# Optimization experiments

Hardware: AMD Instinct MI355X
Metric: run time of the kernel (lower is better)

Reference implementation:

```python
import jax, jax.numpy as jnp
import numpy as np

B, T, F = 32, 64, 128          # batch, time_steps, input_dim
H = 8                           # feat_dim (GRU hidden, MHA embed)
NH, HD = 4, 2                   # num_heads, head_dim
HID = 32                        # hidden_dim (out_proj out-features)


def setup_inputs() -> dict:
    key = jax.random.key(0)
    ks = jax.random.split(key, 16)
    s = 0.1
    inp = {
        'x': jax.random.normal(ks[0], (B, T, F), jnp.float32),
        # input_proj: Linear(F, F)
        'Wp': jax.random.normal(ks[1], (F, F), jnp.float32) * s,
        'bp': jax.random.normal(ks[2], (F,), jnp.float32) * s,
        # per-feature GRU weights stacked over F (input size 1 -> squeeze)
        'W_ih': jax.random.normal(ks[3], (F, 3 * H), jnp.float32) * s,
        'b_ih': jax.random.normal(ks[4], (F, 3 * H), jnp.float32) * s,
        'W_hh': jax.random.normal(ks[5], (F, 3 * H, H), jnp.float32) * s,
        'b_hh': jax.random.normal(ks[6], (F, 3 * H), jnp.float32) * s,
        # shared MultiheadAttention (embed=H, heads=NH)
        'in_w': jax.random.normal(ks[7], (3 * H, H), jnp.float32) * s,
        'in_b': jax.random.normal(ks[8], (3 * H,), jnp.float32) * s,
        'ow': jax.random.normal(ks[9], (H, H), jnp.float32) * s,
        'ob': jax.random.normal(ks[10], (H,), jnp.float32) * s,
        # out_proj: Linear(F*H, HID)
        'Wout': jax.random.normal(ks[11], (HID, F * H), jnp.float32) * s,
        'bout': jax.random.normal(ks[12], (HID,), jnp.float32) * s,
    }
    return inp


def _forward(x, Wp, bp, W_ih, b_ih, W_hh, b_hh, in_w, in_b, ow, ob, Wout, bout):
    xp = x @ Wp.T + bp                               # [B,T,F] input_proj

    # ---- batched per-feature GRU (vectorized over B and F, scan over T) ----
    def step(h, x_t):                                # h [B,F,H], x_t [B,F]
        gx = x_t[..., None] * W_ih + b_ih            # [B,F,3H]
        gh = jnp.einsum('bfh,fgh->bfg', h, W_hh) + b_hh
        r = jax.nn.sigmoid(gx[..., :H] + gh[..., :H])
        z = jax.nn.sigmoid(gx[..., H:2 * H] + gh[..., H:2 * H])
        n = jnp.tanh(gx[..., 2 * H:] + r * gh[..., 2 * H:])
        h_new = (1.0 - z) * n + z * h
        return h_new, h_new

    h0 = jnp.zeros((x.shape[0], F, H), x.dtype)
    _, hs = jax.lax.scan(step, h0, jnp.moveaxis(xp, 1, 0))   # [T,B,F,H]
    out = jnp.moveaxis(hs, 0, 1)                              # [B,T,F,H]

    # ---- shared MHA over time, batched across (B, F) ----
    seq = out.transpose(0, 2, 1, 3)                           # [B,F,T,H]
    qkv = seq @ in_w.T + in_b                                 # [B,F,T,3H]
    q, k, v = jnp.split(qkv, 3, axis=-1)
    def heads(t):  # [B,F,T,H] -> [B,F,T,NH,HD]
        return t.reshape(t.shape[:-1] + (NH, HD))
    q, k, v = heads(q), heads(k), heads(v)
    scale = 1.0 / np.sqrt(HD)
    scores = jnp.einsum('bfqnd,bfknd->bfnqk', q, k) * scale   # [B,F,NH,T,T]
    w = jax.nn.softmax(scores, axis=-1)
    ctx = jnp.einsum('bfnqk,bfknd->bfqnd', w, v)
    ctx = ctx.reshape(ctx.shape[:2] + (ctx.shape[2], H))      # [B,F,T,H]
    attn_out = ctx @ ow.T + ob                                # [B,F,T,H]
    attention = attn_out.transpose(0, 2, 1, 3)                # [B,T,F,H]

    # ---- flatten GRU outputs and project ----
    y = out.reshape(out.shape[0], out.shape[1], F * H) @ Wout.T + bout  # [B,T,HID]
    return y, attention


def reference(x, Wp, bp, W_ih, b_ih, W_hh, b_hh, in_w, in_b, ow, ob, Wout, bout):
    return _forward(x, Wp, bp, W_ih, b_ih, W_hh, b_hh, in_w, in_b, ow, ob, Wout, bout)
```

## Files before the change

### kernel.cpp

```cpp
#include <hip/hip_runtime.h>


namespace {
constexpr int Bb = 32, Tt = 64, Ff = 128, Hh = 8, HIDh = 32;
constexpr int G3H = 24;
constexpr float L2E = 1.44269504088896340736f;
constexpr int XPS  = 0;
constexpr int HOUT = 260;
constexpr int OCT  = 2340;
constexpr int KV   = 4900;
constexpr int SM_SIZE = KV + 4 * 1088;
}

__device__ __forceinline__ float rcp_(float x) {
#if __has_builtin(__builtin_amdgcn_rcpf)
  return __builtin_amdgcn_rcpf(x);
#else
  return 1.0f / x;
#endif
}
__device__ __forceinline__ float exp2_(float x) {
#if __has_builtin(__builtin_amdgcn_exp2f)
  return __builtin_amdgcn_exp2f(x);
#else
  return exp2f(x);
#endif
}

#define MHA_STEP(K0C, K1C, V0C, V1C)                         \
  {                                                          \
    _Pragma("unroll") for (int i = 0; i < 4; ++i) {          \
      float s = fmaf(q0[i], K0C, q1[i] * K1C);               \
      float p = exp2_(s);                                    \
      ps[i] += p;                                            \
      c0[i] = fmaf(p, V0C, c0[i]);                           \
      c1[i] = fmaf(p, V1C, c1[i]);                           \
    }                                                        \
  }

__global__ __launch_bounds__(256, 4) void k_fused(
    const float* __restrict__ x, const float* __restrict__ Wp, const float* __restrict__ bp,
    const float* __restrict__ W_ih, const float* __restrict__ b_ih,
    const float* __restrict__ W_hh, const float* __restrict__ b_hh,
    const float* __restrict__ in_w, const float* __restrict__ in_b,
    const float* __restrict__ ow, const float* __restrict__ ob,
    float* __restrict__ outp, float* __restrict__ attn) {
  __shared__ float smem[SM_SIZE];
  const int tid = threadIdx.x;
  const int t = tid & 63;
  const int w = tid >> 6;
  const int blk = blockIdx.x;
  const int b = blk >> 5;
  const int f0 = (blk & 31) * 4;

  {
    const int f = f0 + w;
    const float4* xr = (const float4*)(x + (b * Tt + t) * Ff);
    const float4* wr = (const float4*)(Wp + f * Ff);
    float acc = bp[f];
#pragma unroll 8
    for (int k = 0; k < Ff / 4; ++k) {
      float4 xv = xr[k], wv = wr[k];
      acc = fmaf(xv.x, wv.x, acc); acc = fmaf(xv.y, wv.y, acc);
      acc = fmaf(xv.z, wv.z, acc); acc = fmaf(xv.w, wv.w, acc);
    }
    smem[XPS + w * 65 + t] = acc;
  }
  __syncthreads();

  if (tid < 32) {
    __builtin_amdgcn_s_setprio(1);
    const int g = t >> 3, j = t & 7;
    const int f = f0 + g;
    const float* wb = W_hh + (f * G3H + j) * Hh;
    const float nL = -L2E, S2 = 2.0f * L2E;
    float w0s[8], w1s[8], w2s[8];
#pragma unroll
    for (int h = 0; h < 8; ++h) {
      w0s[h] = wb[h] * nL;
      w1s[h] = wb[64 + h] * nL;
      w2s[h] = wb[128 + h] * S2;
    }
    const float wi0s = W_ih[f * G3H + j] * nL;
    const float wi1s = W_ih[f * G3H + 8 + j] * nL;
    const float wi2s = W_ih[f * G3H + 16 + j] * S2;
    const float bias_r = (b_ih[f * G3H + j] + b_hh[f * G3H + j]) * nL;
    const float bias_z = (b_ih[f * G3H + 8 + j] + b_hh[f * G3H + 8 + j]) * nL;
    const float bi2s = b_ih[f * G3H + 16 + j] * S2;
    const float bh2s = b_hh[f * G3H + 16 + j] * S2;
    float hall[8];
#pragma unroll
    for (int h = 0; h < 8; ++h) hall[h] = 0.f;
    float h_own = 0.f;
    const int base = t & 56;
    float* hdst = &smem[HOUT + g * 520 + j * 65];
    const float* xps = &smem[XPS + g * 65];
    for (int tt = 0; tt < Tt; ++tt) {
      float xt = xps[tt];
      float a0 = bias_r, a1 = bias_z, a2 = bh2s;
#pragma unroll
      for (int h = 0; h < 8; ++h) {
        a0 = fmaf(hall[h], w0s[h], a0);
        a1 = fmaf(hall[h], w1s[h], a1);
        a2 = fmaf(hall[h], w2s[h], a2);
      }
      float r = rcp_(1.0f + exp2_(fmaf(xt, wi0s, a0)));
      float z = rcp_(1.0f + exp2_(fmaf(xt, wi1s, a1)));
      float narg = fmaf(r, a2, fmaf(xt, wi2s, bi2s));
      float n = fmaf(-2.0f, rcp_(exp2_(narg) + 1.0f), 1.0f);
      float hn = fmaf(z, h_own - n, n);
      hdst[tt] = hn;
      h_own = hn;
#pragma unroll
      for (int h = 0; h < 8; ++h) hall[h] = __shfl(hn, base + h, 64);
    }
    __builtin_amdgcn_s_setprio(0);
  }
  __syncthreads();

  {
    float4* og = (float4*)(outp + (size_t)(b * Ff + f0) * Tt * Hh);
#pragma unroll
    for (int i = 0; i < 2; ++i) {
      int v = i * 256 + tid;
      int fl = v >> 7, rem = v & 127;
      int tt = rem >> 1, j0 = (rem & 1) * 4;
      const float* hp = &smem[HOUT + fl * 520 + j0 * 65 + tt];
      og[v] = make_float4(hp[0], hp[65], hp[130], hp[195]);
    }
  }

  {
    constexpr float SCL = 0.70710678118654752f * L2E;
    const float* hsrc = &smem[HOUT + w * 520];
    float* oc = &smem[OCT + w * 640];
    float* kk0 = &smem[KV + w * 1088];
    float* kk1 = kk0 + 272;
    float* vv0 = kk0 + 544;
    float* vv1 = kk0 + 816;

    float sq[8];
#pragma unroll
    for (int h = 0; h < 8; ++h) sq[h] = hsrc[h * 65 + t];
    float qv[8], ka[8], va[8];
#pragma unroll
    for (int jj = 0; jj < 8; ++jj) {
      float aq = in_b[jj], ak = in_b[8 + jj], av = in_b[16 + jj];
#pragma unroll
      for (int h = 0; h < 8; ++h) {
        aq = fmaf(sq[h], in_w[jj * 8 + h], aq);
        ak = fmaf(sq[h], in_w[(8 + jj) * 8 + h], ak);
        av = fmaf(sq[h], in_w[(16 + jj) * 8 + h], av);
      }
      qv[jj] = aq * SCL; ka[jj] = ak; va[jj] = av;
    }
#pragma unroll
    for (int n = 0; n < 4; ++n) {
      *(float2*)&oc[t * 10 + 2 * n] = make_float2(qv[2 * n], qv[2 * n + 1]);
      kk0[n * 68 + t] = ka[2 * n];
      kk1[n * 68 + t] = ka[2 * n + 1];
      vv0[n * 68 + t] = va[2 * n];
      vv1[n * 68 + t] = va[2 * n + 1];
    }
    asm volatile("s_waitcnt lgkmcnt(0)" ::: "memory");

    const int n = t >> 4, qq = t & 15;
    float q0[4], q1[4];
#pragma unroll
    for (int i = 0; i < 4; ++i) {
      float2 qp = *(const float2*)&oc[(qq + 16 * i) * 10 + 2 * n];
      q0[i] = qp.x; q1[i] = qp.y;
    }
    float ps[4], c0[4], c1[4];
#pragma unroll
    for (int i = 0; i < 4; ++i) { ps[i] = 0.f; c0[i] = 0.f; c1[i] = 0.f; }
#pragma unroll 2
    for (int kt4 = 0; kt4 < Tt; kt4 += 4) {
      float4 k0 = *(const float4*)&kk0[n * 68 + kt4];
      float4 k1 = *(const float4*)&kk1[n * 68 + kt4];
      float4 v0 = *(const float4*)&vv0[n * 68 + kt4];
      float4 v1 = *(const float4*)&vv1[n * 68 + kt4];
      MHA_STEP(k0.x, k1.x, v0.x, v1.x)
      MHA_STEP(k0.y, k1.y, v0.y, v1.y)
      MHA_STEP(k0.z, k1.z, v0.z, v1.z)
      MHA_STEP(k0.w, k1.w, v0.w, v1.w)
    }
#pragma unroll
    for (int i = 0; i < 4; ++i) {
      float inv = rcp_(ps[i]);
      *(float2*)&oc[(qq + 16 * i) * 10 + 2 * n] =
          make_float2(c0[i] * inv, c1[i] * inv);
    }
    asm volatile("s_waitcnt lgkmcnt(0)" ::: "memory");

    {
      float2 cp0 = *(const float2*)&oc[t * 10 + 0];
      float2 cp1 = *(const float2*)&oc[t * 10 + 2];
      float2 cp2 = *(const float2*)&oc[t * 10 + 4];
      float2 cp3 = *(const float2*)&oc[t * 10 + 6];
      float cx[8] = {cp0.x, cp0.y, cp1.x, cp1.y, cp2.x, cp2.y, cp3.x, cp3.y};
      float o8[8];
#pragma unroll
      for (int jj = 0; jj < 8; ++jj) {
        float a = ob[jj];
#pragma unroll
        for (int h = 0; h < 8; ++h) a = fmaf(cx[h], ow[jj * 8 + h], a);
        o8[jj] = a;
      }
      *(float2*)&oc[t * 10 + 0] = make_float2(o8[0], o8[1]);
      *(float2*)&oc[t * 10 + 2] = make_float2(o8[2], o8[3]);
      *(float2*)&oc[t * 10 + 4] = make_float2(o8[4], o8[5]);
      *(float2*)&oc[t * 10 + 6] = make_float2(o8[6], o8[7]);
    }
  }
  __syncthreads();

  {
#pragma unroll
    for (int i = 0; i < 2; ++i) {
      int v = i * 256 + tid;
      int tt = v >> 3, c = v & 7;
      int fl = c >> 1, h0 = (c & 1) * 4;
      const float* sp = &smem[OCT + fl * 640 + tt * 10 + h0];
      float4 val = make_float4(sp[0], sp[1], sp[2], sp[3]);
      *(float4*)(attn + (((size_t)b * Tt + tt) * Ff + f0 + fl) * Hh + h0) = val;
    }
  }
}

__global__ __launch_bounds__(128) void k_outproj(
    const float* __restrict__ outp, const float* __restrict__ Wout,
    const float* __restrict__ bout, float* __restrict__ y) {
  constexpr int TT = 8;
  int blk = blockIdx.x;
  int b = blk >> 3;
  int t0 = (blk & 7) * TT;
  int tid = threadIdx.x;
  int oq = tid >> 4;
  int fc = tid & 15;
  float acc[TT][4];
#pragma unroll
  for (int tt = 0; tt < TT; ++tt)
#pragma unroll
    for (int od = 0; od < 4; ++od) acc[tt][od] = 0.f;
#pragma unroll
  for (int ff = 0; ff < 8; ++ff) {
    int f = fc * 8 + ff;
    const float4* rb = (const float4*)(outp + ((b * Ff + f) * Tt + t0) * Hh);
    float4 rv[16];
#pragma unroll
    for (int i = 0; i < 16; ++i) rv[i] = rb[i];
#pragma unroll
    for (int od = 0; od < 4; ++od) {
      int o = oq * 4 + od;
      const float4* wbp = (const float4*)(Wout + o * (Ff * Hh) + f * Hh);
      float4 wa = wbp[0], wc = wbp[1];
#pragma unroll
      for (int tt = 0; tt < TT; ++tt) {
        float4 ra = rv[tt * 2], rc = rv[tt * 2 + 1];
        float s = acc[tt][od];
        s = fmaf(ra.x, wa.x, s); s = fmaf(ra.y, wa.y, s);
        s = fmaf(ra.z, wa.z, s); s = fmaf(ra.w, wa.w, s);
        s = fmaf(rc.x, wc.x, s); s = fmaf(rc.y, wc.y, s);
        s = fmaf(rc.z, wc.z, s); s = fmaf(rc.w, wc.w, s);
        acc[tt][od] = s;
      }
    }
  }
#pragma unroll
  for (int tt = 0; tt < TT; ++tt)
#pragma unroll
    for (int od = 0; od < 4; ++od) {
      float v = acc[tt][od];
      v += __shfl_xor(v, 1, 16);
      v += __shfl_xor(v, 2, 16);
      v += __shfl_xor(v, 4, 16);
      v += __shfl_xor(v, 8, 16);
      acc[tt][od] = v;
    }
#pragma unroll
  for (int tt = 0; tt < TT; ++tt) {
    if (fc == tt) {
#pragma unroll
      for (int od = 0; od < 4; ++od) {
        int o = oq * 4 + od;
        y[(b * Tt + t0 + tt) * HIDh + o] = acc[tt][od] + bout[o];
      }
    }
  }
}

extern "C" void kernel_launch(void* const* d_in, const int* in_sizes, int n_in,
                              void* d_out, int out_size, void* d_ws, size_t ws_size,
                              hipStream_t stream) {
  (void)in_sizes; (void)n_in; (void)out_size; (void)ws_size;
  const float* x    = (const float*)d_in[0];
  const float* Wp   = (const float*)d_in[1];
  const float* bp   = (const float*)d_in[2];
  const float* W_ih = (const float*)d_in[3];
  const float* b_ih = (const float*)d_in[4];
  const float* W_hh = (const float*)d_in[5];
  const float* b_hh = (const float*)d_in[6];
  const float* in_w = (const float*)d_in[7];
  const float* in_b = (const float*)d_in[8];
  const float* ow   = (const float*)d_in[9];
  const float* ob   = (const float*)d_in[10];
  const float* Wout = (const float*)d_in[11];
  const float* bout = (const float*)d_in[12];

  float* y    = (float*)d_out;
  float* attn = (float*)d_out + Bb * Tt * HIDh;
  float* outp = (float*)d_ws;

  hipLaunchKernelGGL(k_fused, dim3(Bb * (Ff / 4)), dim3(256), 0, stream,
                     x, Wp, bp, W_ih, b_ih, W_hh, b_hh, in_w, in_b, ow, ob, outp, attn);
  hipLaunchKernelGGL(k_outproj, dim3(Bb * (Tt / 8)), dim3(128), 0, stream,
                     outp, Wout, bout, y);
}
```

Before: 61.93 us.

## Fuse output projection into main kernel via atomic accumulation

```diff
diff --git a/kernel.cpp b/kernel.cpp
--- a/kernel.cpp
+++ b/kernel.cpp
@@ -44,7 +44,8 @@
     const float* __restrict__ W_hh, const float* __restrict__ b_hh,
     const float* __restrict__ in_w, const float* __restrict__ in_b,
     const float* __restrict__ ow, const float* __restrict__ ob,
-    float* __restrict__ outp, float* __restrict__ attn) {
+    const float* __restrict__ Wout, const float* __restrict__ bout,
+    float* __restrict__ y, float* __restrict__ attn) {
   __shared__ float smem[SM_SIZE];
   const int tid = threadIdx.x;
   const int t = tid & 63;
@@ -119,15 +120,34 @@
   __syncthreads();
 
   {
-    float4* og = (float4*)(outp + (size_t)(b * Ff + f0) * Tt * Hh);
-#pragma unroll
-    for (int i = 0; i < 2; ++i) {
-      int v = i * 256 + tid;
-      int fl = v >> 7, rem = v & 127;
-      int tt = rem >> 1, j0 = (rem & 1) * 4;
-      const float* hp = &smem[HOUT + fl * 520 + j0 * 65 + tt];
-      og[v] = make_float4(hp[0], hp[65], hp[130], hp[195]);
-    }
+    const int od0 = w * 8;
+    float part[8];
+#pragma unroll
+    for (int od = 0; od < 8; ++od) part[od] = 0.f;
+#pragma unroll
+    for (int fl = 0; fl < 4; ++fl) {
+      float hv[8];
+#pragma unroll
+      for (int h = 0; h < 8; ++h) hv[h] = smem[HOUT + fl * 520 + h * 65 + t];
+#pragma unroll
+      for (int od = 0; od < 8; ++od) {
+        const float4* wq = (const float4*)(Wout + (od0 + od) * (Ff * Hh) + (f0 + fl) * Hh);
+        float4 wa = wq[0], wb4 = wq[1];
+        float s = part[od];
+        s = fmaf(hv[0], wa.x, s);  s = fmaf(hv[1], wa.y, s);
+        s = fmaf(hv[2], wa.z, s);  s = fmaf(hv[3], wa.w, s);
+        s = fmaf(hv[4], wb4.x, s); s = fmaf(hv[5], wb4.y, s);
+        s = fmaf(hv[6], wb4.z, s); s = fmaf(hv[7], wb4.w, s);
+        part[od] = s;
+      }
+    }
+    if ((blk & 31) == 0) {
+#pragma unroll
+      for (int od = 0; od < 8; ++od) part[od] += bout[od0 + od];
+    }
+    float* yb = y + ((size_t)b * Tt + t) * HIDh + od0;
+#pragma unroll
+    for (int od = 0; od < 8; ++od) atomicAdd(&yb[od], part[od]);
   }
 
   {
@@ -228,72 +248,10 @@
   }
 }
 
-__global__ __launch_bounds__(128) void k_outproj(
-    const float* __restrict__ outp, const float* __restrict__ Wout,
-    const float* __restrict__ bout, float* __restrict__ y) {
-  constexpr int TT = 8;
-  int blk = blockIdx.x;
-  int b = blk >> 3;
-  int t0 = (blk & 7) * TT;
-  int tid = threadIdx.x;
-  int oq = tid >> 4;
-  int fc = tid & 15;
-  float acc[TT][4];
-#pragma unroll
-  for (int tt = 0; tt < TT; ++tt)
-#pragma unroll
-    for (int od = 0; od < 4; ++od) acc[tt][od] = 0.f;
-#pragma unroll
-  for (int ff = 0; ff < 8; ++ff) {
-    int f = fc * 8 + ff;
-    const float4* rb = (const float4*)(outp + ((b * Ff + f) * Tt + t0) * Hh);
-    float4 rv[16];
-#pragma unroll
-    for (int i = 0; i < 16; ++i) rv[i] = rb[i];
-#pragma unroll
-    for (int od = 0; od < 4; ++od) {
-      int o = oq * 4 + od;
-      const float4* wbp = (const float4*)(Wout + o * (Ff * Hh) + f * Hh);
-      float4 wa = wbp[0], wc = wbp[1];
-#pragma unroll
-      for (int tt = 0; tt < TT; ++tt) {
-        float4 ra = rv[tt * 2], rc = rv[tt * 2 + 1];
-        float s = acc[tt][od];
-        s = fmaf(ra.x, wa.x, s); s = fmaf(ra.y, wa.y, s);
-        s = fmaf(ra.z, wa.z, s); s = fmaf(ra.w, wa.w, s);
-        s = fmaf(rc.x, wc.x, s); s = fmaf(rc.y, wc.y, s);
-        s = fmaf(rc.z, wc.z, s); s = fmaf(rc.w, wc.w, s);
-        acc[tt][od] = s;
-      }
-    }
-  }
-#pragma unroll
-  for (int tt = 0; tt < TT; ++tt)
-#pragma unroll
-    for (int od = 0; od < 4; ++od) {
-      float v = acc[tt][od];
-      v += __shfl_xor(v, 1, 16);
-      v += __shfl_xor(v, 2, 16);
-      v += __shfl_xor(v, 4, 16);
-      v += __shfl_xor(v, 8, 16);
-      acc[tt][od] = v;
-    }
-#pragma unroll
-  for (int tt = 0; tt < TT; ++tt) {
-    if (fc == tt) {
-#pragma unroll
-      for (int od = 0; od < 4; ++od) {
-        int o = oq * 4 + od;
-        y[(b * Tt + t0 + tt) * HIDh + o] = acc[tt][od] + bout[o];
-      }
-    }
-  }
-}
-
 extern "C" void kernel_launch(void* const* d_in, const int* in_sizes, int n_in,
                               void* d_out, int out_size, void* d_ws, size_t ws_size,
                               hipStream_t stream) {
-  (void)in_sizes; (void)n_in; (void)out_size; (void)ws_size;
+  (void)in_sizes; (void)n_in; (void)out_size; (void)d_ws; (void)ws_size;
   const float* x    = (const float*)d_in[0];
   const float* Wp   = (const float*)d_in[1];
   const float* bp   = (const float*)d_in[2];
@@ -310,10 +268,10 @@
 
   float* y    = (float*)d_out;
   float* attn = (float*)d_out + Bb * Tt * HIDh;
-  float* outp = (float*)d_ws;
+
+  hipMemsetAsync(y, 0, (size_t)Bb * Tt * HIDh * sizeof(float), stream);
 
   hipLaunchKernelGGL(k_fused, dim3(Bb * (Ff / 4)), dim3(256), 0, stream,
-                     x, Wp, bp, W_ih, b_ih, W_hh, b_hh, in_w, in_b, ow, ob, outp, attn);
-  hipLaunchKernelGGL(k_outproj, dim3(Bb * (Tt / 8)), dim3(128), 0, stream,
-                     outp, Wout, bout, y);
-}
+                     x, Wp, bp, W_ih, b_ih, W_hh, b_hh, in_w, in_b, ow, ob,
+                     Wout, bout, y, attn);
+}
```

Result: slower. 131.0 us (+111.5%).
